# Kernel optimization log

Measured on AMD Instinct MI355X. Metric: run time of the kernel, lower is better.

## Reference

```python
import jax, jax.numpy as jnp
import numpy as np

SHAPES = [(64, 64), (32, 32), (16, 16), (8, 8)]  # (H, W) per level, sum HW = 5440
DIMS, NH, NLVL, NPTS, D_HEIGHT, NCAM, NQ, BS = 256, 8, 4, 8, 4, 6, 10000, 1


def ms_deform_attn(value, shapes, loc, attw):
    # value [B, sumHW, nH, dh]; loc [B, nq, nH, L, P, 2] in [0,1]; attw [B, nq, nH, L, P]
    B, _, nH, dh = value.shape
    nq, P = loc.shape[1], loc.shape[4]
    out = jnp.zeros((B, nH, nq, dh), value.dtype)
    start = 0
    for lvl, (h, w) in enumerate(shapes):
        v = value[:, start:start + h * w].transpose(0, 2, 1, 3)  # [B,nH,hw,dh]
        start += h * w
        l = loc[:, :, :, lvl].transpose(0, 2, 1, 3, 4)  # [B,nH,nq,P,2]
        x = l[..., 0] * w - 0.5
        y = l[..., 1] * h - 0.5
        x0, y0 = jnp.floor(x), jnp.floor(y)
        acc = jnp.zeros((B, nH, nq, P, dh), value.dtype)
        for dy in (0.0, 1.0):
            for dx in (0.0, 1.0):
                cx, cy = x0 + dx, y0 + dy
                wgt = (1.0 - jnp.abs(x - cx)) * (1.0 - jnp.abs(y - cy))
                valid = (cx >= 0) & (cx < w) & (cy >= 0) & (cy < h)
                xi = jnp.clip(cx, 0, w - 1).astype(jnp.int32)
                yi = jnp.clip(cy, 0, h - 1).astype(jnp.int32)
                idx = (yi * w + xi).reshape(B, nH, -1)  # [B,nH,nq*P]
                g = jnp.take_along_axis(v, idx[..., None], axis=2).reshape(B, nH, nq, P, dh)
                acc = acc + jnp.where(valid, wgt, 0.0)[..., None] * g
        aw = attw[:, :, :, lvl].transpose(0, 2, 1, 3)  # [B,nH,nq,P]
        out = out + jnp.einsum('bhqp,bhqpd->bhqd', aw, acc)
    return out.transpose(0, 2, 1, 3).reshape(B, nq, nH * dh)


def setup_inputs() -> dict:
    key = jax.random.key(0)
    ks = jax.random.split(key, 16)
    l = sum(h * w for h, w in SHAPES)
    s = 1.0 / np.sqrt(DIMS)
    inp = {
        'query': jax.random.normal(ks[0], (BS, NQ, DIMS), jnp.float32),
        'key': jax.random.normal(ks[1], (NCAM, l, BS, DIMS), jnp.float32),
        'value': jax.random.normal(ks[2], (NCAM, l, BS, DIMS), jnp.float32),
        'ref_points': jax.random.uniform(ks[3], (NCAM, BS, NQ, D_HEIGHT, 2), jnp.float32),
        'vox_mask': jax.random.randint(ks[4], (NCAM, BS, NQ, D_HEIGHT), 0, 2) > 0,
        'spatial_shapes': np.array(SHAPES, dtype=np.int64),
        'level_start_index': np.array([0, 4096, 5120, 5376], dtype=np.int64),
        'value_W': jax.random.uniform(ks[5], (DIMS, DIMS), jnp.float32, -s, s),
        'value_b': jnp.zeros((DIMS,), jnp.float32),
        'off_W': jax.random.normal(ks[6], (DIMS, NH * NLVL * NPTS * 2), jnp.float32) * 0.01,
        'off_b': jax.random.normal(ks[7], (NH * NLVL * NPTS * 2,), jnp.float32) * 0.1,
        'attw_W': jax.random.normal(ks[8], (DIMS, NH * NLVL * NPTS), jnp.float32) * 0.02,
        'attw_b': jnp.zeros((NH * NLVL * NPTS,), jnp.float32),
        'out_W': jax.random.uniform(ks[9], (DIMS, DIMS), jnp.float32, -s, s),
        'out_b': jnp.zeros((DIMS,), jnp.float32),
    }
    return inp


def reference(query, key, value, ref_points, vox_mask, spatial_shapes, level_start_index,
              value_W, value_b, off_W, off_b, attw_W, attw_b, out_W, out_b):
    shapes = [(int(h), int(w)) for h, w in np.asarray(spatial_shapes)]
    bs, nq, dims = query.shape
    cam = vox_mask.shape[0]
    B = bs * cam
    nH = NH
    dh = dims // nH
    Lv, P, D = len(shapes), NPTS, ref_points.shape[3]

    # value_proj; key unused by deformable attention math
    v = value.transpose(2, 0, 1, 3).reshape(B, -1, dims)
    v = (v @ value_W + value_b).reshape(B, -1, nH, dh)

    # rebatch: every camera sees the full (batch-0 visible) query set; padded
    # entries in the original are discarded, so computing all and masking is exact.
    q = jnp.broadcast_to(query[:, None], (bs, cam, nq, dims)).reshape(B, nq, dims)

    off = (q @ off_W + off_b).reshape(B, nq, nH, Lv, P, 2)
    attw = jax.nn.softmax((q @ attw_W + attw_b).reshape(B, nq, nH, Lv * P), -1)
    attw = attw.reshape(B, nq, nH, Lv, P)

    norm = jnp.array([[w, h] for h, w in shapes], q.dtype)  # [Lv,2] -> (W,H)
    off = off / norm[None, None, None, :, None, :]

    ref_rb = ref_points.transpose(1, 0, 2, 3, 4).reshape(B, nq, D, 2)
    off = off.reshape(B, nq, nH, Lv, P // D, D, 2)
    loc = (ref_rb[:, :, None, None, None] + off).reshape(B, nq, nH, Lv, P, 2)

    out = ms_deform_attn(v, shapes, loc, attw).reshape(bs, cam, nq, dims)

    valid = (vox_mask[:, 0].sum(-1) > 0).astype(q.dtype)  # [cam,nq] (batch-0 indexes, as original)
    slots = jnp.einsum('cq,bcqd->bqd', valid, out)
    count = (vox_mask.sum(-1) > 0).transpose(1, 2, 0).sum(-1).astype(q.dtype)
    count = jnp.maximum(count, 1.0)
    slots = slots / count[..., None]
    slots = slots @ out_W + out_b
    return slots + query  # dropout = identity (eval); inp_residual = query
```

## Files before the change

### kernel.cpp

```cpp
#include <hip/hip_runtime.h>


typedef unsigned short ushort_t;
typedef unsigned int uint_t;
typedef __attribute__((ext_vector_type(8))) short bf16x8;
typedef __attribute__((ext_vector_type(4))) float f32x4;
typedef __attribute__((ext_vector_type(2))) _Float16 f16x2;

__device__ __forceinline__ float bf2f(ushort_t u) {
    return __uint_as_float(((uint_t)u) << 16);
}
__device__ __forceinline__ ushort_t f2bf(float f) {
    uint_t i = __float_as_uint(f);
    uint_t r = i + 0x7fffu + ((i >> 16) & 1u);
    return (ushort_t)(r >> 16);
}
__device__ __forceinline__ bf16x8 pack8(float4 v0, float4 v1) {
    union { uint_t u[4]; bf16x8 v; } r;
    asm("v_cvt_pk_bf16_f32 %0, %1, %2" : "=v"(r.u[0]) : "v"(v0.x), "v"(v0.y));
    asm("v_cvt_pk_bf16_f32 %0, %1, %2" : "=v"(r.u[1]) : "v"(v0.z), "v"(v0.w));
    asm("v_cvt_pk_bf16_f32 %0, %1, %2" : "=v"(r.u[2]) : "v"(v1.x), "v"(v1.y));
    asm("v_cvt_pk_bf16_f32 %0, %1, %2" : "=v"(r.u[3]) : "v"(v1.z), "v"(v1.w));
    return r.v;
}
__device__ __forceinline__ ushort_t f2h(float f) {
    union { _Float16 h; ushort_t u; } cv;
    cv.h = (_Float16)f;
    return cv.u;
}

__device__ __forceinline__ void pk_fma8(uint_t* a, uint_t wp, const uint4& v) {
    asm("v_pk_fma_f16 %0, %1, %2, %0" : "+v"(a[0]) : "v"(wp), "v"(v.x));
    asm("v_pk_fma_f16 %0, %1, %2, %0" : "+v"(a[1]) : "v"(wp), "v"(v.y));
    asm("v_pk_fma_f16 %0, %1, %2, %0" : "+v"(a[2]) : "v"(wp), "v"(v.z));
    asm("v_pk_fma_f16 %0, %1, %2, %0" : "+v"(a[3]) : "v"(wp), "v"(v.w));
}

__global__ __launch_bounds__(256) void prep_w(
    const float* __restrict__ Wv, const float* __restrict__ Wo,
    const float* __restrict__ Wf, const float* __restrict__ Wa,
    ushort_t* __restrict__ Tv, ushort_t* __restrict__ To,
    ushort_t* __restrict__ Tqk) {
    const int z = blockIdx.z;
    const float* W;
    ushort_t* T;
    int N;
    if (z == 0)      { W = Wv; T = Tv;              N = 256; }
    else if (z == 1) { W = Wo; T = To;              N = 256; }
    else if (z == 2) { W = Wf; T = Tqk;             N = 512; }
    else             { W = Wa; T = Tqk + 512 * 256; N = 256; }
    const int n0 = blockIdx.y * 32;
    if (n0 >= N) return;
    const int k0 = blockIdx.x * 32;

    __shared__ float tile[32][33];
    const int tx = threadIdx.x & 31;
    const int ty = threadIdx.x >> 5;
    #pragma unroll
    for (int r = 0; r < 4; ++r) {
        const int k = ty + r * 8;
        tile[k][tx] = W[(size_t)(k0 + k) * N + n0 + tx];
    }
    __syncthreads();
    #pragma unroll
    for (int r = 0; r < 4; ++r) {
        const int n = ty + r * 8;
        T[(size_t)(n0 + n) * 256 + k0 + tx] = f2bf(tile[tx][n]);
    }
}

template <bool AF32, int OUT_MODE, bool RESID>
__device__ __forceinline__ void gemm_body(
    ushort_t (*sA)[128][32], ushort_t (*sB)[128][32],
    const void* __restrict__ Av, int Astride, const ushort_t* __restrict__ Wt,
    const float* __restrict__ bias0, const float* __restrict__ bias1, int split,
    const float* __restrict__ resid, void* __restrict__ Cv,
    int M, int N, int bx, int by) {
    const int m0 = bx * 128;
    const int n0 = by * 128;
    const int t    = threadIdx.x;
    const int lane = t & 63;
    const int w    = t >> 6;
    const int wr   = w >> 1, wc = w & 1;

    const int srow = t >> 2;
    const int skof = (t & 3) * 8;

    const bool am0 = (m0 + srow) < M;
    const bool am1 = (m0 + 64 + srow) < M;
    const float*    Af0 = (const float*)Av + (size_t)(m0 + srow) * Astride + skof;
    const float*    Af1 = Af0 + (size_t)64 * Astride;
    const ushort_t* Ab0 = (const ushort_t*)Av + (size_t)(m0 + srow) * Astride + skof;
    const ushort_t* Ab1 = Ab0 + (size_t)64 * Astride;
    const ushort_t* Bp0 = Wt + (size_t)(n0 + srow) * 256 + skof;
    const ushort_t* Bp1 = Bp0 + (size_t)64 * 256;

    const bf16x8 zz = {0, 0, 0, 0, 0, 0, 0, 0};

    auto loadA = [&](const float* af, const ushort_t* ab, int ko, bool ok) -> bf16x8 {
        if (!ok) return zz;
        if (AF32) {
            const float4 v0 = *(const float4*)(af + ko);
            const float4 v1 = *(const float4*)(af + ko + 4);
            return pack8(v0, v1);
        }
        return *(const bf16x8*)(ab + ko);
    };

    f32x4 acc[4][4];
    #pragma unroll
    for (int i = 0; i < 4; ++i)
        #pragma unroll
        for (int j = 0; j < 4; ++j)
            acc[i][j] = (f32x4){0.f, 0.f, 0.f, 0.f};

    {
        const bf16x8 a0 = loadA(Af0, Ab0, 0, am0);
        const bf16x8 a1 = loadA(Af1, Ab1, 0, am1);
        const bf16x8 b0 = *(const bf16x8*)(Bp0);
        const bf16x8 b1 = *(const bf16x8*)(Bp1);
        *(bf16x8*)(&sA[0][srow][skof])      = a0;
        *(bf16x8*)(&sA[0][64 + srow][skof]) = a1;
        *(bf16x8*)(&sB[0][srow][skof])      = b0;
        *(bf16x8*)(&sB[0][64 + srow][skof]) = b1;
    }
    __syncthreads();

    const int rl = lane & 15;
    const int kq = (lane >> 4) * 8;

    for (int k = 0; k < 8; ++k) {
        const int buf = k & 1;

        bf16x8 na0 = zz, na1 = zz, nb0 = zz, nb1 = zz;
        if (k < 7) {
            const int ko = (k + 1) * 32;
            na0 = loadA(Af0, Ab0, ko, am0);
            na1 = loadA(Af1, Ab1, ko, am1);
            nb0 = *(const bf16x8*)(Bp0 + ko);
            nb1 = *(const bf16x8*)(Bp1 + ko);
        }

        bf16x8 af[4], bfr[4];
        #pragma unroll
        for (int i = 0; i < 4; ++i)
            af[i] = *(const bf16x8*)(&sA[buf][wr * 64 + i * 16 + rl][kq]);
        #pragma unroll
        for (int j = 0; j < 4; ++j)
            bfr[j] = *(const bf16x8*)(&sB[buf][wc * 64 + j * 16 + rl][kq]);
        #pragma unroll
        for (int i = 0; i < 4; ++i)
            #pragma unroll
            for (int j = 0; j < 4; ++j)
                acc[i][j] = __builtin_amdgcn_mfma_f32_16x16x32_bf16(
                    af[i], bfr[j], acc[i][j], 0, 0, 0);

        if (k < 7) {
            __syncthreads();
            *(bf16x8*)(&sA[buf ^ 1][srow][skof])      = na0;
            *(bf16x8*)(&sA[buf ^ 1][64 + srow][skof]) = na1;
            *(bf16x8*)(&sB[buf ^ 1][srow][skof])      = nb0;
            *(bf16x8*)(&sB[buf ^ 1][64 + srow][skof]) = nb1;
            __syncthreads();
        }
    }

    const int col_l = lane & 15;
    const int rq    = (lane >> 4) * 4;
    #pragma unroll
    for (int j = 0; j < 4; ++j) {
        const int gn = n0 + wc * 64 + j * 16 + col_l;
        const float bj = (gn < split) ? bias0[gn] : bias1[gn - split];
        #pragma unroll
        for (int i = 0; i < 4; ++i) {
            #pragma unroll
            for (int r = 0; r < 4; ++r) {
                const int gm = m0 + wr * 64 + i * 16 + rq + r;
                if (gm >= M) continue;
                float v = acc[i][j][r] + bj;
                if (RESID) v += resid[(size_t)gm * N + gn];
                if (OUT_MODE == 1)
                    ((ushort_t*)Cv)[(size_t)gm * N + gn] = f2bf(v);
                else if (OUT_MODE == 2)
                    ((ushort_t*)Cv)[(size_t)gm * N + gn] = f2h(v);
                else
                    ((float*)Cv)[(size_t)gm * N + gn] = v;
            }
        }
    }
}

__global__ __launch_bounds__(256) void gemm_vqk(
    const float* __restrict__ value, const ushort_t* __restrict__ value_Wt,
    const float* __restrict__ value_b, ushort_t* __restrict__ vproj,
    const float* __restrict__ query, const ushort_t* __restrict__ qk_Wt,
    const float* __restrict__ off_b, const float* __restrict__ attw_b,
    ushort_t* __restrict__ qkcat) {
    __shared__ ushort_t sA[2][128][32];
    __shared__ ushort_t sB[2][128][32];
    int b = blockIdx.x;
    if (b < 510) {
        gemm_body<true, 2, false>(sA, sB, value, 256, value_Wt, value_b,
                                  value_b, 256, nullptr, (void*)vproj,
                                  32640, 256, b % 255, b / 255);
    } else {
        b -= 510;
        gemm_body<true, 1, false>(sA, sB, query, 256, qk_Wt, off_b, attw_b,
                                  512, nullptr, (void*)qkcat, 10000, 768,
                                  b % 79, b / 79);
    }
}

__global__ __launch_bounds__(256) void gemm_out_k(
    const ushort_t* __restrict__ slots,
    const ushort_t* __restrict__ out_Wt,
    const float* __restrict__ out_b, const float* __restrict__ query,
    float* __restrict__ out) {
    __shared__ ushort_t sA[2][128][32];
    __shared__ ushort_t sB[2][128][32];
    gemm_body<false, 0, true>(sA, sB, slots, 768, out_Wt, out_b, out_b, 256,
                              query, (void*)out, 10000, 256,
                              blockIdx.x, blockIdx.y);
}

__global__ __launch_bounds__(256) void sample_k(
    ushort_t* __restrict__ qkcat,
    const float* __restrict__ refp,
    const int* __restrict__ vox,
    const ushort_t* __restrict__ vproj) {
    const int q   = blockIdx.x;
    const int tid = threadIdx.x;
    const int lane  = tid & 63;
    const int h     = tid >> 5;
    const int lp    = tid & 31;
    const int slice = (tid >> 2) & 7;
    const int g     = tid & 3;

    __shared__ float s_valid[8];
    __shared__ float s_red[256][8];

    if (tid < 6) {
        const int base = (tid * 10000 + q) * 4;
        const int mm = vox[base] | vox[base + 1] | vox[base + 2] | vox[base + 3];
        s_valid[tid] = mm ? 1.0f : 0.0f;
    }

    const float a = bf2f(qkcat[(size_t)q * 768 + 512 + tid]);
    float mx = a;
    #pragma unroll
    for (int o = 16; o >= 1; o >>= 1) mx = fmaxf(mx, __shfl_xor(mx, o));
    const float e = __expf(a - mx);
    float se = e;
    #pragma unroll
    for (int o = 16; o >= 1; o >>= 1) se += __shfl_xor(se, o);
    const float aw = e / se;

    const int lvl = lp >> 3;
    const int p   = lp & 7;
    const int dd  = p & 3;
    const int   Sarr[4]   = {64, 32, 16, 8};
    const int   Lstart[4] = {0, 4096, 5120, 5376};
    const int   S  = Sarr[lvl];
    const float Sf = (float)S;
    const int   lstart = Lstart[lvl];
    const int   hoff   = h << 6;
    const float ox = bf2f(qkcat[(size_t)q * 768 + h * 64 + lvl * 16 + p * 2 + 0]) / Sf;
    const float oy = bf2f(qkcat[(size_t)q * 768 + h * 64 + lvl * 16 + p * 2 + 1]) / Sf;

    __syncthreads();
    float sv[6];
    #pragma unroll
    for (int c = 0; c < 6; ++c) sv[c] = s_valid[c];
    const float cnt = sv[0] + sv[1] + sv[2] + sv[3] + sv[4] + sv[5];

    float acc[8] = {0.f, 0.f, 0.f, 0.f, 0.f, 0.f, 0.f, 0.f};
    const char* vpb = (const char*)vproj;
    const int goff = g << 4;
    const int srcbase = (lane & 32) + slice * 4;

    for (int c = 0; c < 6; ++c) {
        if (sv[c] == 0.0f) continue;

        int    cb[4];
        uint_t cwp[4];
        {
            const int cbase = c * 5440 + lstart;
            const int rbase = ((c * 10000 + q) * 4 + dd) * 2;
            const float rx = refp[rbase + 0];
            const float ry = refp[rbase + 1];
            const float x  = (rx + ox) * Sf - 0.5f;
            const float y  = (ry + oy) * Sf - 0.5f;
            const float x0 = floorf(x), y0 = floorf(y);
            #pragma unroll
            for (int k = 0; k < 4; ++k) {
                const float cx = x0 + (float)(k & 1);
                const float cy = y0 + (float)(k >> 1);
                const float wgt = (1.0f - fabsf(x - cx)) * (1.0f - fabsf(y - cy));
                const bool ok = (cx >= 0.0f) & (cx < Sf) & (cy >= 0.0f) & (cy < Sf);
                const int xi = (int)fminf(fmaxf(cx, 0.0f), Sf - 1.0f);
                const int yi = (int)fminf(fmaxf(cy, 0.0f), Sf - 1.0f);
                cb[k] = ((cbase + yi * S + xi) << 9) + hoff;
                const float cw = ok ? wgt * aw : 0.0f;
                const uint_t hw = (uint_t)f2h(cw);
                cwp[k] = (hw << 16) | hw;
            }
        }

        int b[4][4];
        #pragma unroll
        for (int j = 0; j < 4; ++j) {
            const int src = srcbase + j;
            b[j][0] = __shfl(cb[0], src);
            b[j][1] = __shfl(cb[1], src);
            b[j][2] = __shfl(cb[2], src);
            b[j][3] = __shfl(cb[3], src);
        }

        uint_t acch[4] = {0u, 0u, 0u, 0u};
        uint4 v0 = *(const uint4*)(vpb + (b[0][0] + goff));
        uint4 v1 = *(const uint4*)(vpb + (b[0][1] + goff));
        uint4 v2 = *(const uint4*)(vpb + (b[0][2] + goff));
        uint4 v3 = *(const uint4*)(vpb + (b[0][3] + goff));
        #pragma unroll
        for (int j = 0; j < 4; ++j) {
            uint4 n0 = v0, n1 = v1, n2 = v2, n3 = v3;
            if (j < 3) {
                n0 = *(const uint4*)(vpb + (b[j + 1][0] + goff));
                n1 = *(const uint4*)(vpb + (b[j + 1][1] + goff));
                n2 = *(const uint4*)(vpb + (b[j + 1][2] + goff));
                n3 = *(const uint4*)(vpb + (b[j + 1][3] + goff));
            }
            const int src = srcbase + j;
            const uint_t w0 = (uint_t)__shfl((int)cwp[0], src);
            const uint_t w1 = (uint_t)__shfl((int)cwp[1], src);
            const uint_t w2 = (uint_t)__shfl((int)cwp[2], src);
            const uint_t w3 = (uint_t)__shfl((int)cwp[3], src);
            pk_fma8(acch, w0, v0);
            pk_fma8(acch, w1, v1);
            pk_fma8(acch, w2, v2);
            pk_fma8(acch, w3, v3);
            v0 = n0; v1 = n1; v2 = n2; v3 = n3;
        }

        #pragma unroll
        for (int n = 0; n < 4; ++n) {
            union { uint_t u; f16x2 h; } cvu;
            cvu.u = acch[n];
            acc[2 * n]     += (float)cvu.h.x;
            acc[2 * n + 1] += (float)cvu.h.y;
        }
    }

    #pragma unroll
    for (int n = 0; n < 8; ++n) s_red[tid][n] = acc[n];
    __syncthreads();

    const int cch = tid & 31;
    float sum = 0.0f;
    #pragma unroll
    for (int s = 0; s < 8; ++s)
        sum += s_red[h * 32 + s * 4 + (cch >> 3)][cch & 7];

    qkcat[(size_t)q * 768 + 512 + tid] = f2bf(sum / fmaxf(cnt, 1.0f));
}

extern "C" void kernel_launch(void* const* d_in, const int* in_sizes, int n_in,
                              void* d_out, int out_size, void* d_ws, size_t ws_size,
                              hipStream_t stream) {
    const float* query   = (const float*)d_in[0];
    const float* value   = (const float*)d_in[2];
    const float* refp    = (const float*)d_in[3];
    const int*   vox     = (const int*)d_in[4];
    const float* value_W = (const float*)d_in[7];
    const float* value_b = (const float*)d_in[8];
    const float* off_W   = (const float*)d_in[9];
    const float* off_b   = (const float*)d_in[10];
    const float* attw_W  = (const float*)d_in[11];
    const float* attw_b  = (const float*)d_in[12];
    const float* out_W   = (const float*)d_in[13];
    const float* out_b   = (const float*)d_in[14];
    float* out = (float*)d_out;

    char* ws = (char*)d_ws;
    ushort_t* vproj    = (ushort_t*)ws;
    ushort_t* qkcat    = (ushort_t*)(ws + 16711680);
    ushort_t* value_Wt = (ushort_t*)(ws + 32071680);
    ushort_t* out_Wt   = (ushort_t*)(ws + 32071680 + 131072);
    ushort_t* qk_Wt    = (ushort_t*)(ws + 32071680 + 262144);

    prep_w<<<dim3(8, 16, 4), 256, 0, stream>>>(
        value_W, out_W, off_W, attw_W, value_Wt, out_Wt, qk_Wt);
    gemm_vqk<<<984, 256, 0, stream>>>(value, value_Wt, value_b, vproj,
                                      query, qk_Wt, off_b, attw_b, qkcat);
    sample_k<<<10000, 256, 0, stream>>>(qkcat, refp, vox, vproj);
    gemm_out_k<<<dim3(79, 2), 256, 0, stream>>>(qkcat + 512, out_Wt, out_b,
                                                query, out);
}
```

Measured before the change: 333.1 us.

## Split sampling blocks per head group and replace shared-memory reductions with shuffles

The sampling kernel now launches two 128-thread blocks per query, each handling four heads, instead of one 256-thread block. Every wave computes the camera-valid mask itself through a vector load and lane shuffles, and the final reduction across the eight slices uses xor-shuffles instead of a shared-memory buffer, so both __syncthreads barriers and the LDS are gone. One lane per slice group then writes eight bf16 outputs in a single 16-byte store. The intent is to cut barrier stalls and LDS traffic and raise occupancy, at the cost of twice as many blocks and the mask load being repeated in every wave.

```diff
diff --git a/kernel.cpp b/kernel.cpp
--- a/kernel.cpp
+++ b/kernel.cpp
@@ -223,29 +223,31 @@
                               blockIdx.x, blockIdx.y);
 }
 
-__global__ __launch_bounds__(256) void sample_k(
+__global__ __launch_bounds__(128) void sample_k(
     ushort_t* __restrict__ qkcat,
     const float* __restrict__ refp,
     const int* __restrict__ vox,
     const ushort_t* __restrict__ vproj) {
-    const int q   = blockIdx.x;
-    const int tid = threadIdx.x;
-    const int lane  = tid & 63;
-    const int h     = tid >> 5;
-    const int lp    = tid & 31;
+    const int q    = blockIdx.x;
+    const int hb   = blockIdx.y << 2;
+    const int tid  = threadIdx.x;
+    const int lane = tid & 63;
+    const int h    = hb + (tid >> 5);
+    const int lp   = tid & 31;
     const int slice = (tid >> 2) & 7;
     const int g     = tid & 3;
 
-    __shared__ float s_valid[8];
-    __shared__ float s_red[256][8];
-
-    if (tid < 6) {
-        const int base = (tid * 10000 + q) * 4;
-        const int mm = vox[base] | vox[base + 1] | vox[base + 2] | vox[base + 3];
-        s_valid[tid] = mm ? 1.0f : 0.0f;
-    }
-
-    const float a = bf2f(qkcat[(size_t)q * 768 + 512 + tid]);
+    int mm = 0;
+    if (lane < 6) {
+        const uint4 vm = *(const uint4*)(vox + ((lane * 10000 + q) << 2));
+        mm = (int)(vm.x | vm.y | vm.z | vm.w);
+    }
+    float sv[6];
+    #pragma unroll
+    for (int c = 0; c < 6; ++c) sv[c] = __shfl(mm, c) ? 1.0f : 0.0f;
+    const float cnt = sv[0] + sv[1] + sv[2] + sv[3] + sv[4] + sv[5];
+
+    const float a = bf2f(qkcat[(size_t)q * 768 + 512 + h * 32 + lp]);
     float mx = a;
     #pragma unroll
     for (int o = 16; o >= 1; o >>= 1) mx = fmaxf(mx, __shfl_xor(mx, o));
@@ -266,12 +268,6 @@
     const int   hoff   = h << 6;
     const float ox = bf2f(qkcat[(size_t)q * 768 + h * 64 + lvl * 16 + p * 2 + 0]) / Sf;
     const float oy = bf2f(qkcat[(size_t)q * 768 + h * 64 + lvl * 16 + p * 2 + 1]) / Sf;
-
-    __syncthreads();
-    float sv[6];
-    #pragma unroll
-    for (int c = 0; c < 6; ++c) sv[c] = s_valid[c];
-    const float cnt = sv[0] + sv[1] + sv[2] + sv[3] + sv[4] + sv[5];
 
     float acc[8] = {0.f, 0.f, 0.f, 0.f, 0.f, 0.f, 0.f, 0.f};
     const char* vpb = (const char*)vproj;
@@ -352,16 +348,25 @@
     }
 
     #pragma unroll
-    for (int n = 0; n < 8; ++n) s_red[tid][n] = acc[n];
-    __syncthreads();
-
-    const int cch = tid & 31;
-    float sum = 0.0f;
-    #pragma unroll
-    for (int s = 0; s < 8; ++s)
-        sum += s_red[h * 32 + s * 4 + (cch >> 3)][cch & 7];
-
-    qkcat[(size_t)q * 768 + 512 + tid] = f2bf(sum / fmaxf(cnt, 1.0f));
+    for (int n = 0; n < 8; ++n) {
+        acc[n] += __shfl_xor(acc[n], 4);
+        acc[n] += __shfl_xor(acc[n], 8);
+        acc[n] += __shfl_xor(acc[n], 16);
+    }
+
+    if (slice == 0) {
+        const float inv = 1.0f / fmaxf(cnt, 1.0f);
+        uint4 r;
+        asm("v_cvt_pk_bf16_f32 %0, %1, %2"
+            : "=v"(r.x) : "v"(acc[0] * inv), "v"(acc[1] * inv));
+        asm("v_cvt_pk_bf16_f32 %0, %1, %2"
+            : "=v"(r.y) : "v"(acc[2] * inv), "v"(acc[3] * inv));
+        asm("v_cvt_pk_bf16_f32 %0, %1, %2"
+            : "=v"(r.z) : "v"(acc[4] * inv), "v"(acc[5] * inv));
+        asm("v_cvt_pk_bf16_f32 %0, %1, %2"
+            : "=v"(r.w) : "v"(acc[6] * inv), "v"(acc[7] * inv));
+        *(uint4*)(&qkcat[(size_t)q * 768 + 512 + h * 32 + g * 8]) = r;
+    }
 }
 
 extern "C" void kernel_launch(void* const* d_in, const int* in_sizes, int n_in,
@@ -392,7 +397,7 @@
         value_W, out_W, off_W, attw_W, value_Wt, out_Wt, qk_Wt);
     gemm_vqk<<<984, 256, 0, stream>>>(value, value_Wt, value_b, vproj,
                                       query, qk_Wt, off_b, attw_b, qkcat);
-    sample_k<<<10000, 256, 0, stream>>>(qkcat, refp, vox, vproj);
+    sample_k<<<dim3(10000, 2), 128, 0, stream>>>(qkcat, refp, vox, vproj);
     gemm_out_k<<<dim3(79, 2), 256, 0, stream>>>(qkcat + 512, out_Wt, out_b,
                                                 query, out);
 }
```

Result: faster. 325.8 us (-2.2%).
